# Kernel optimization log

Measured on AMD Instinct MI355X. Metric: run time of the kernel, lower is better.

Reference implementation:

```python
import jax, jax.numpy as jnp
import numpy as np

N, LQ, C, M, L, P = 8, 2048, 256, 8, 4, 4
DH = C // M  # 32
LENS = (2048, 1024, 512, 256)


def setup_inputs() -> dict:
    key = jax.random.key(0)
    ks = jax.random.split(key, 8)
    s = 1.0 / np.sqrt(C)
    return {
        "query": jax.random.normal(ks[0], (N, LQ, C), jnp.float32),
        "reference_points": jax.random.uniform(ks[1], (N, LQ, L, 1), jnp.float32),
        "input_flatten": jax.random.normal(ks[2], (N, sum(LENS), C), jnp.float32),
        "temporal_lens": np.array(LENS, np.int64),
        "level_start_index": np.array([0, 2048, 3072, 3584], np.int64),
        "W_off": jax.random.normal(ks[3], (C, M * L * P), jnp.float32) * 0.01,
        "b_off": jax.random.normal(ks[4], (M * L * P,), jnp.float32),
        "W_attn": jax.random.normal(ks[5], (C, M * L * P), jnp.float32) * 0.01,
        "b_attn": jnp.zeros((M * L * P,), jnp.float32),
        "W_val": jax.random.normal(ks[6], (C, C), jnp.float32) * s,
        "b_val": jnp.zeros((C,), jnp.float32),
        "W_out": jax.random.normal(ks[7], (C, C), jnp.float32) * s,
        "b_out": jnp.zeros((C,), jnp.float32),
    }


def _deform_core(value, lens, loc, attn):
    # value: (N, S, M, DH); loc, attn: (N, LQ, M, L, P); loc in normalized [0,1] coords.
    # Equivalent to per-level F.grid_sample (bilinear, zeros padding, align_corners=False)
    # on a 1xT image: pixel position = loc*T - 0.5; the y-coord 0.5 lands exactly on row 0.
    outs = []
    start = 0
    for l, T in enumerate(lens):
        v = value[:, start:start + T].transpose(0, 2, 1, 3)  # (N, M, T, DH)
        start += T
        pos = loc[..., l, :] * T - 0.5                       # (N, LQ, M, P)
        x0f = jnp.floor(pos)
        frac = pos - x0f
        x0 = x0f.astype(jnp.int32)

        def gather(idx):
            i = jnp.clip(idx, 0, T - 1).transpose(0, 2, 1, 3).reshape(N, M, LQ * P, 1)
            return jnp.take_along_axis(v, i, axis=2).reshape(N, M, LQ, P, DH)

        in0 = ((x0 >= 0) & (x0 < T)).astype(value.dtype)
        in1 = ((x0 + 1 >= 0) & (x0 + 1 < T)).astype(value.dtype)
        w0 = ((1.0 - frac) * in0).transpose(0, 2, 1, 3)[..., None]  # (N, M, LQ, P, 1)
        w1 = (frac * in1).transpose(0, 2, 1, 3)[..., None]
        outs.append(gather(x0) * w0 + gather(x0 + 1) * w1)          # (N, M, LQ, P, DH)
    sampled = jnp.stack(outs, axis=3)          # (N, M, LQ, L, P, DH)
    aw = attn.transpose(0, 2, 1, 3, 4)         # (N, M, LQ, L, P)
    return jnp.einsum('nmqlpd,nmqlp->nqmd', sampled, aw).reshape(N, LQ, C)


def reference(query, reference_points, input_flatten, temporal_lens, level_start_index,
              W_off, b_off, W_attn, b_attn, W_val, b_val, W_out, b_out):
    lens = [int(t) for t in np.asarray(temporal_lens)[:L]]  # static per-level lengths
    value = (input_flatten @ W_val + b_val).reshape(N, -1, M, DH)
    off = (query @ W_off + b_off).reshape(N, LQ, M, L, P)
    attn = jax.nn.softmax((query @ W_attn + b_attn).reshape(N, LQ, M, L * P), axis=-1)
    attn = attn.reshape(N, LQ, M, L, P)
    norm = jnp.asarray(lens, query.dtype)                    # offset_normalizer (L,)
    loc = reference_points[:, :, None, :, None, 0] + off / norm[None, None, None, :, None]
    out = _deform_core(value, lens, loc, attn)
    out = out @ W_out + b_out
    return out, loc, attn
```

## Files before the change

### kernel.cpp

```cpp
#include <hip/hip_runtime.h>
#include <hip/hip_bf16.h>
#include <math.h>

#define NB 8
#define LQ 2048
#define SSUM 3840

typedef unsigned short ushort_t;
typedef unsigned int uint_t;
typedef __attribute__((ext_vector_type(8))) short bf16x8;
typedef __attribute__((ext_vector_type(4))) float f32x4;

__device__ __forceinline__ ushort_t f2bf(float f) {
  __hip_bfloat16 h = __float2bfloat16(f);
  return *reinterpret_cast<ushort_t*>(&h);
}
__device__ __forceinline__ uint_t pk2bf(float lo, float hi) {
  float2 t; t.x = lo; t.y = hi;
  __hip_bfloat162 h = __float22bfloat162_rn(t);
  return *reinterpret_cast<uint_t*>(&h);
}
__device__ __forceinline__ float bf2f_lo(uint_t u) {
  union { uint_t u32; float f; } x;
  x.u32 = u << 16;
  return x.f;
}
__device__ __forceinline__ float bf2f_hi(uint_t u) {
  union { uint_t u32; float f; } x;
  x.u32 = u & 0xffff0000u;
  return x.f;
}
__device__ __forceinline__ void ld_lds16(const void* g, void* l) {
  __builtin_amdgcn_global_load_lds(
      (const __attribute__((address_space(1))) void*)g,
      (__attribute__((address_space(3))) void*)l, 16, 0, 0);
}

__global__ __launch_bounds__(256) void prep(
    const float* __restrict__ W_val, const float* __restrict__ W_off,
    const float* __restrict__ W_attn, const float* __restrict__ W_out,
    ushort_t* __restrict__ BtVal, ushort_t* __restrict__ BtOA,
    ushort_t* __restrict__ BtOut) {
  const int b = blockIdx.x, t = threadIdx.x;
  if (b < 256) { BtVal[b * 256 + t] = f2bf(W_val[(size_t)t * 256 + b]); return; }
  if (b < 512) { int n = b - 256; BtOut[n * 256 + t] = f2bf(W_out[(size_t)t * 256 + n]); return; }
  if (b < 640) { int n = b - 512; BtOA[n * 256 + t] = f2bf(W_off[(size_t)t * 128 + n]); return; }
  int n = b - 640; BtOA[(128 + n) * 256 + t] = f2bf(W_attn[(size_t)t * 128 + n]);
}

template <bool AF32>
__global__ __launch_bounds__(256) void gemm_fused(
    int job_base,
    const float* __restrict__ in_flat, const float* __restrict__ query,
    const ushort_t* __restrict__ core,
    const ushort_t* __restrict__ BtVal, const ushort_t* __restrict__ BtOA,
    const ushort_t* __restrict__ BtOut,
    const float* __restrict__ b_val, const float* __restrict__ b_off,
    const float* __restrict__ b_attn, const float* __restrict__ b_out,
    ushort_t* __restrict__ value, float* __restrict__ loc,
    float* __restrict__ attn, float* __restrict__ out) {
  __shared__ ushort_t Ab[2][64][32];
  __shared__ ushort_t Bb[2][256][32];

  const int job = job_base + blockIdx.x;

  const float* Afp = nullptr;
  const ushort_t* Abf = nullptr;
  const ushort_t* Bt;
  const float* bias_lo; const float* bias_hi;
  int bm, cstride;
  ushort_t* Cb = nullptr;
  float* Cf_lo = nullptr; float* Cf_hi = nullptr;

  if (job < 480) {
    bm = job * 64; Afp = in_flat; Bt = BtVal;
    bias_lo = b_val; bias_hi = b_val + 128; Cb = value; cstride = 256;
  } else if (job < 736) {
    bm = (job - 480) * 64; Afp = query; Bt = BtOA;
    bias_lo = b_off; bias_hi = b_attn; Cf_lo = loc; Cf_hi = attn; cstride = 128;
  } else {
    bm = (job - 736) * 64; Abf = core; Bt = BtOut;
    bias_lo = b_out; bias_hi = b_out + 128; Cf_lo = out; Cf_hi = out + 128;
    cstride = 256;
  }

  const int tid = threadIdx.x;
  const int lane = tid & 63;
  const int wv = tid >> 6;
  const int quad = lane >> 4;
  const int l16 = lane & 15;
  const int wm = (wv >> 1) * 32;
  const int wn = (wv & 1) * 128;
  const int drow = lane >> 2;
  const int dk = (lane & 3) * 8;

  const int asr = tid >> 2;
  const int ask = (tid & 3) * 8;

  f32x4 acc[2][8];
#pragma unroll
  for (int i = 0; i < 2; ++i)
#pragma unroll
    for (int j = 0; j < 8; ++j) acc[i][j] = (f32x4)(0.f);

  auto stageB = [&](int db, int k0) {
#pragma unroll
    for (int c = 0; c < 4; ++c)
      ld_lds16(Bt + (size_t)(wv * 64 + c * 16 + drow) * 256 + k0 + dk,
               &Bb[db][wv * 64 + c * 16 + drow][dk]);
  };
  auto stageA_dma = [&](int db, int k0) {
    ld_lds16(Abf + (size_t)(bm + wv * 16 + drow) * 256 + k0 + dk,
             &Ab[db][wv * 16 + drow][dk]);
  };
  auto stageA_f32 = [&](int db, int k0) {
    const float* gp = Afp + (size_t)(bm + asr) * 256 + k0 + ask;
    float4 f0 = *(const float4*)gp;
    float4 f1 = *(const float4*)(gp + 4);
    uint4 c;
    c.x = pk2bf(f0.x, f0.y);
    c.y = pk2bf(f0.z, f0.w);
    c.z = pk2bf(f1.x, f1.y);
    c.w = pk2bf(f1.z, f1.w);
    *(uint4*)&Ab[db][asr][ask] = c;
  };

  if (AF32) stageA_f32(0, 0); else stageA_dma(0, 0);
  stageB(0, 0);

#pragma unroll
  for (int it = 0; it < 8; ++it) {
    const int db = it & 1;
    __syncthreads();
    if (it < 7) {
      if (AF32) stageA_f32(db ^ 1, (it + 1) * 32); else stageA_dma(db ^ 1, (it + 1) * 32);
      stageB(db ^ 1, (it + 1) * 32);
    }
    bf16x8 af[2], bfr[8];
#pragma unroll
    for (int mi = 0; mi < 2; ++mi)
      af[mi] = *(const bf16x8*)&Ab[db][wm + mi * 16 + l16][quad * 8];
#pragma unroll
    for (int ni = 0; ni < 8; ++ni)
      bfr[ni] = *(const bf16x8*)&Bb[db][wn + ni * 16 + l16][quad * 8];
#pragma unroll
    for (int mi = 0; mi < 2; ++mi)
#pragma unroll
      for (int ni = 0; ni < 8; ++ni)
        acc[mi][ni] = __builtin_amdgcn_mfma_f32_16x16x32_bf16(af[mi], bfr[ni], acc[mi][ni], 0, 0, 0);
  }

  const int hi = wv & 1;
  const float* bias = hi ? bias_hi : bias_lo;
  ushort_t* Cbw = Cb ? (Cb + (hi ? 128 : 0)) : nullptr;
  float* Cfw = hi ? Cf_hi : Cf_lo;

#pragma unroll
  for (int ni = 0; ni < 8; ++ni) {
    int cc = ni * 16 + l16;
    float bv = bias[cc];
#pragma unroll
    for (int mi = 0; mi < 2; ++mi) {
      f32x4 v = acc[mi][ni];
      int rbase = bm + wm + mi * 16 + quad * 4;
#pragma unroll
      for (int r = 0; r < 4; ++r) {
        float o = v[r] + bv;
        size_t idx = (size_t)(rbase + r) * cstride + cc;
        if (Cbw) Cbw[idx] = f2bf(o);
        else     Cfw[idx] = o;
      }
    }
  }
}

__global__ __launch_bounds__(256) void deform_fused(
    const ushort_t* __restrict__ value,
    float* __restrict__ locbuf,
    float* __restrict__ attnbuf,
    const float* __restrict__ refp,
    ushort_t* __restrict__ core) {
  const int tid = threadIdx.x;
  const int nq0 = blockIdx.x * 4;
  const int n = nq0 >> 11;

  __shared__ float slv[512];
  __shared__ float slog[512];
  __shared__ float4 sp[512];

  const float rnorm[4] = {1.f / 2048.f, 1.f / 1024.f, 1.f / 512.f, 1.f / 256.f};
  const int lensA[4] = {2048, 1024, 512, 256};
  const int startsA[4] = {0, 2048, 3072, 3584};

#pragma unroll
  for (int j = 0; j < 2; ++j) {
    int s = tid + j * 256;
    int q = s >> 7;
    int r = s & 127;
    int l = (r >> 2) & 3;
    float lv = refp[(size_t)(nq0 + q) * 4 + l] +
               locbuf[(size_t)nq0 * 128 + s] * rnorm[l];
    locbuf[(size_t)nq0 * 128 + s] = lv;
    slv[s] = lv;
    slog[s] = attnbuf[(size_t)nq0 * 128 + s];
  }
  __syncthreads();

  if (tid < 32) {
    int base = tid * 16;
    float v[16];
#pragma unroll
    for (int i = 0; i < 16; ++i) v[i] = slog[base + i];
    float mx = v[0];
#pragma unroll
    for (int i = 1; i < 16; ++i) mx = fmaxf(mx, v[i]);
    float ssum = 0.f;
#pragma unroll
    for (int i = 0; i < 16; ++i) { v[i] = __expf(v[i] - mx); ssum += v[i]; }
    float rs = 1.f / ssum;
    float* gout = attnbuf + (size_t)nq0 * 128 + base;
#pragma unroll
    for (int i = 0; i < 16; ++i) {
      float pv = v[i] * rs;
      slog[base + i] = pv;
      gout[i] = pv;
    }
  }
  __syncthreads();

#pragma unroll
  for (int j = 0; j < 2; ++j) {
    int s = tid + j * 256;
    int q = s >> 7;
    int r = s & 127;
    int m = r >> 4;
    int lp = r & 15;
    int l = lp >> 2;
    int T = lensA[l];
    float lv = slv[s];
    float aw = slog[s];
    float pos = lv * (float)T - 0.5f;
    float x0f = floorf(pos);
    float fr = pos - x0f;
    int x0 = (int)x0f;
    float w0 = ((unsigned)x0 < (unsigned)T) ? (1.f - fr) * aw : 0.f;
    float w1 = ((unsigned)(x0 + 1) < (unsigned)T) ? fr * aw : 0.f;
    int i0 = min(max(x0, 0), T - 1);
    int i1 = min(max(x0 + 1, 0), T - 1);
    float4 pr;
    pr.x = w0;
    pr.y = w1;
    pr.z = __int_as_float((startsA[l] + i0) * 256);
    pr.w = __int_as_float((startsA[l] + i1) * 256);
    sp[q * 128 + lp * 8 + m] = pr;
  }
  __syncthreads();

  const int q = tid >> 6;
  const int t64 = tid & 63;
  const int m = t64 >> 3;
  const int g = t64 & 7;
  const ushort_t* vbase = value + (size_t)n * (SSUM * 256) + m * 32 + g * 4;

  float a0 = 0.f, a1 = 0.f, a2 = 0.f, a3 = 0.f;
#pragma unroll
  for (int lp = 0; lp < 16; ++lp) {
    float4 pr = sp[q * 128 + lp * 8 + m];
    int o0 = __float_as_int(pr.z);
    int o1 = __float_as_int(pr.w);
    uint2 u0 = *(const uint2*)(vbase + o0);
    uint2 u1 = *(const uint2*)(vbase + o1);
    a0 += pr.x * bf2f_lo(u0.x) + pr.y * bf2f_lo(u1.x);
    a1 += pr.x * bf2f_hi(u0.x) + pr.y * bf2f_hi(u1.x);
    a2 += pr.x * bf2f_lo(u0.y) + pr.y * bf2f_lo(u1.y);
    a3 += pr.x * bf2f_hi(u0.y) + pr.y * bf2f_hi(u1.y);
  }
  uint2 outp;
  outp.x = (uint_t)f2bf(a0) | ((uint_t)f2bf(a1) << 16);
  outp.y = (uint_t)f2bf(a2) | ((uint_t)f2bf(a3) << 16);
  *(uint2*)&core[(size_t)(nq0 + q) * 256 + m * 32 + g * 4] = outp;
}

extern "C" void kernel_launch(void* const* d_in, const int* in_sizes, int n_in,
                              void* d_out, int out_size, void* d_ws, size_t ws_size,
                              hipStream_t stream) {
  const float* query    = (const float*)d_in[0];
  const float* refpts   = (const float*)d_in[1];
  const float* in_flat  = (const float*)d_in[2];
  const float* W_off  = (const float*)d_in[5];
  const float* b_off  = (const float*)d_in[6];
  const float* W_attn = (const float*)d_in[7];
  const float* b_attn = (const float*)d_in[8];
  const float* W_val  = (const float*)d_in[9];
  const float* b_val  = (const float*)d_in[10];
  const float* W_out  = (const float*)d_in[11];
  const float* b_out  = (const float*)d_in[12];

  float* out  = (float*)d_out;
  float* loc  = out + (size_t)NB * LQ * 256;
  float* attn = loc + (size_t)NB * LQ * 128;

  ushort_t* value = (ushort_t*)d_ws;
  ushort_t* core  = value + (size_t)NB * SSUM * 256;
  ushort_t* BtVal = core + (size_t)NB * LQ * 256;
  ushort_t* BtOA  = BtVal + 65536;
  ushort_t* BtOut = BtOA + 65536;

  const int Mq = NB * LQ;

  prep<<<768, 256, 0, stream>>>(W_val, W_off, W_attn, W_out, BtVal, BtOA, BtOut);

  gemm_fused<true><<<736, 256, 0, stream>>>(
      0, in_flat, query, core, BtVal, BtOA, BtOut,
      b_val, b_off, b_attn, b_out, value, loc, attn, out);

  deform_fused<<<Mq / 4, 256, 0, stream>>>(value, loc, attn, refpts, core);

  gemm_fused<false><<<256, 256, 0, stream>>>(
      736, in_flat, query, core, BtVal, BtOA, BtOut,
      b_val, b_off, b_attn, b_out, value, loc, attn, out);
}
```

Measured before the change: 164.7 us.

## Fuse loc/softmax epilogue into GEMM and XOR-swizzle LDS tiles

Moves the sampling-location computation (reference point plus normalized offset) and the per-head softmax of attention logits into the epilogue of the offset/attention GEMM. The softmax uses wave shuffles across the 16 columns of each head. This removes a global read-modify-write pass and two barriers from the deform kernel. It also applies an XOR swizzle to the LDS layout of the A and B tiles to reduce bank conflicts on the MFMA fragment loads. The trade-off is more shuffles and exp work in the GEMM epilogue and more complex address math.

```diff
diff --git a/kernel.cpp b/kernel.cpp
--- a/kernel.cpp
+++ b/kernel.cpp
@@ -57,6 +57,7 @@
     const ushort_t* __restrict__ BtOut,
     const float* __restrict__ b_val, const float* __restrict__ b_off,
     const float* __restrict__ b_attn, const float* __restrict__ b_out,
+    const float* __restrict__ refp,
     ushort_t* __restrict__ value, float* __restrict__ loc,
     float* __restrict__ attn, float* __restrict__ out) {
   __shared__ ushort_t Ab[2][64][32];
@@ -68,17 +69,20 @@
   const ushort_t* Abf = nullptr;
   const ushort_t* Bt;
   const float* bias_lo; const float* bias_hi;
-  int bm, cstride;
+  int bm, cstride, jt;
   ushort_t* Cb = nullptr;
   float* Cf_lo = nullptr; float* Cf_hi = nullptr;
 
   if (job < 480) {
+    jt = 0;
     bm = job * 64; Afp = in_flat; Bt = BtVal;
     bias_lo = b_val; bias_hi = b_val + 128; Cb = value; cstride = 256;
   } else if (job < 736) {
+    jt = 1;
     bm = (job - 480) * 64; Afp = query; Bt = BtOA;
     bias_lo = b_off; bias_hi = b_attn; Cf_lo = loc; Cf_hi = attn; cstride = 128;
   } else {
+    jt = 2;
     bm = (job - 736) * 64; Abf = core; Bt = BtOut;
     bias_lo = b_out; bias_hi = b_out + 128; Cf_lo = out; Cf_hi = out + 128;
     cstride = 256;
@@ -93,9 +97,13 @@
   const int wn = (wv & 1) * 128;
   const int drow = lane >> 2;
   const int dk = (lane & 3) * 8;
+  const int dks = (((lane & 3) ^ ((drow >> 1) & 3)) * 8);
 
   const int asr = tid >> 2;
   const int ask = (tid & 3) * 8;
+  const int askw = (((tid & 3) ^ ((asr >> 1) & 3)) * 8);
+
+  const int qk = ((quad ^ ((l16 >> 1) & 3)) * 8);
 
   f32x4 acc[2][8];
 #pragma unroll
@@ -106,11 +114,11 @@
   auto stageB = [&](int db, int k0) {
 #pragma unroll
     for (int c = 0; c < 4; ++c)
-      ld_lds16(Bt + (size_t)(wv * 64 + c * 16 + drow) * 256 + k0 + dk,
+      ld_lds16(Bt + (size_t)(wv * 64 + c * 16 + drow) * 256 + k0 + dks,
                &Bb[db][wv * 64 + c * 16 + drow][dk]);
   };
   auto stageA_dma = [&](int db, int k0) {
-    ld_lds16(Abf + (size_t)(bm + wv * 16 + drow) * 256 + k0 + dk,
+    ld_lds16(Abf + (size_t)(bm + wv * 16 + drow) * 256 + k0 + dks,
              &Ab[db][wv * 16 + drow][dk]);
   };
   auto stageA_f32 = [&](int db, int k0) {
@@ -122,7 +130,7 @@
     c.y = pk2bf(f0.z, f0.w);
     c.z = pk2bf(f1.x, f1.y);
     c.w = pk2bf(f1.z, f1.w);
-    *(uint4*)&Ab[db][asr][ask] = c;
+    *(uint4*)&Ab[db][asr][askw] = c;
   };
 
   if (AF32) stageA_f32(0, 0); else stageA_dma(0, 0);
@@ -139,10 +147,10 @@
     bf16x8 af[2], bfr[8];
 #pragma unroll
     for (int mi = 0; mi < 2; ++mi)
-      af[mi] = *(const bf16x8*)&Ab[db][wm + mi * 16 + l16][quad * 8];
+      af[mi] = *(const bf16x8*)&Ab[db][wm + mi * 16 + l16][qk];
 #pragma unroll
     for (int ni = 0; ni < 8; ++ni)
-      bfr[ni] = *(const bf16x8*)&Bb[db][wn + ni * 16 + l16][quad * 8];
+      bfr[ni] = *(const bf16x8*)&Bb[db][wn + ni * 16 + l16][qk];
 #pragma unroll
     for (int mi = 0; mi < 2; ++mi)
 #pragma unroll
@@ -152,81 +160,86 @@
 
   const int hi = wv & 1;
   const float* bias = hi ? bias_hi : bias_lo;
-  ushort_t* Cbw = Cb ? (Cb + (hi ? 128 : 0)) : nullptr;
-  float* Cfw = hi ? Cf_hi : Cf_lo;
-
-#pragma unroll
-  for (int ni = 0; ni < 8; ++ni) {
-    int cc = ni * 16 + l16;
-    float bv = bias[cc];
-#pragma unroll
-    for (int mi = 0; mi < 2; ++mi) {
-      f32x4 v = acc[mi][ni];
-      int rbase = bm + wm + mi * 16 + quad * 4;
-#pragma unroll
-      for (int r = 0; r < 4; ++r) {
-        float o = v[r] + bv;
-        size_t idx = (size_t)(rbase + r) * cstride + cc;
-        if (Cbw) Cbw[idx] = f2bf(o);
-        else     Cfw[idx] = o;
+
+  if (jt == 1) {
+    if (!hi) {
+      const int l = l16 >> 2;
+      const float rn = (float)(1 << l) * (1.0f / 2048.0f);
+#pragma unroll
+      for (int mi = 0; mi < 2; ++mi) {
+        int rbase = bm + wm + mi * 16 + quad * 4;
+#pragma unroll
+        for (int r = 0; r < 4; ++r) {
+          int row = rbase + r;
+          float rp = refp[(size_t)row * 4 + l];
+#pragma unroll
+          for (int ni = 0; ni < 8; ++ni) {
+            int cc = ni * 16 + l16;
+            float o = acc[mi][ni][r] + bias[cc];
+            loc[(size_t)row * 128 + cc] = fmaf(o, rn, rp);
+          }
+        }
+      }
+    } else {
+#pragma unroll
+      for (int mi = 0; mi < 2; ++mi) {
+        int rbase = bm + wm + mi * 16 + quad * 4;
+#pragma unroll
+        for (int r = 0; r < 4; ++r) {
+          int row = rbase + r;
+#pragma unroll
+          for (int ni = 0; ni < 8; ++ni) {
+            int cc = ni * 16 + l16;
+            float x = acc[mi][ni][r] + bias[cc];
+            float mx = x;
+            mx = fmaxf(mx, __shfl_xor(mx, 1, 64));
+            mx = fmaxf(mx, __shfl_xor(mx, 2, 64));
+            mx = fmaxf(mx, __shfl_xor(mx, 4, 64));
+            mx = fmaxf(mx, __shfl_xor(mx, 8, 64));
+            float e = __expf(x - mx);
+            float sm = e;
+            sm += __shfl_xor(sm, 1, 64);
+            sm += __shfl_xor(sm, 2, 64);
+            sm += __shfl_xor(sm, 4, 64);
+            sm += __shfl_xor(sm, 8, 64);
+            attn[(size_t)row * 128 + cc] = e / sm;
+          }
+        }
       }
     }
+  } else {
+    ushort_t* Cbw = Cb ? (Cb + (hi ? 128 : 0)) : nullptr;
+    float* Cfw = hi ? Cf_hi : Cf_lo;
+#pragma unroll
+    for (int ni = 0; ni < 8; ++ni) {
+      int cc = ni * 16 + l16;
+      float bv = bias[cc];
+#pragma unroll
+      for (int mi = 0; mi < 2; ++mi) {
+        f32x4 v = acc[mi][ni];
+        int rbase = bm + wm + mi * 16 + quad * 4;
+#pragma unroll
+        for (int r = 0; r < 4; ++r) {
+          float o = v[r] + bv;
+          size_t idx = (size_t)(rbase + r) * cstride + cc;
+          if (Cbw) Cbw[idx] = f2bf(o);
+          else     Cfw[idx] = o;
+        }
+      }
+    }
   }
 }
 
 __global__ __launch_bounds__(256) void deform_fused(
     const ushort_t* __restrict__ value,
-    float* __restrict__ locbuf,
-    float* __restrict__ attnbuf,
-    const float* __restrict__ refp,
+    const float* __restrict__ locbuf,
+    const float* __restrict__ attnbuf,
     ushort_t* __restrict__ core) {
   const int tid = threadIdx.x;
   const int nq0 = blockIdx.x * 4;
   const int n = nq0 >> 11;
 
-  __shared__ float slv[512];
-  __shared__ float slog[512];
   __shared__ float4 sp[512];
-
-  const float rnorm[4] = {1.f / 2048.f, 1.f / 1024.f, 1.f / 512.f, 1.f / 256.f};
-  const int lensA[4] = {2048, 1024, 512, 256};
-  const int startsA[4] = {0, 2048, 3072, 3584};
-
-#pragma unroll
-  for (int j = 0; j < 2; ++j) {
-    int s = tid + j * 256;
-    int q = s >> 7;
-    int r = s & 127;
-    int l = (r >> 2) & 3;
-    float lv = refp[(size_t)(nq0 + q) * 4 + l] +
-               locbuf[(size_t)nq0 * 128 + s] * rnorm[l];
-    locbuf[(size_t)nq0 * 128 + s] = lv;
-    slv[s] = lv;
-    slog[s] = attnbuf[(size_t)nq0 * 128 + s];
-  }
-  __syncthreads();
-
-  if (tid < 32) {
-    int base = tid * 16;
-    float v[16];
-#pragma unroll
-    for (int i = 0; i < 16; ++i) v[i] = slog[base + i];
-    float mx = v[0];
-#pragma unroll
-    for (int i = 1; i < 16; ++i) mx = fmaxf(mx, v[i]);
-    float ssum = 0.f;
-#pragma unroll
-    for (int i = 0; i < 16; ++i) { v[i] = __expf(v[i] - mx); ssum += v[i]; }
-    float rs = 1.f / ssum;
-    float* gout = attnbuf + (size_t)nq0 * 128 + base;
-#pragma unroll
-    for (int i = 0; i < 16; ++i) {
-      float pv = v[i] * rs;
-      slog[base + i] = pv;
-      gout[i] = pv;
-    }
-  }
-  __syncthreads();
 
 #pragma unroll
   for (int j = 0; j < 2; ++j) {
@@ -236,9 +249,10 @@
     int m = r >> 4;
     int lp = r & 15;
     int l = lp >> 2;
-    int T = lensA[l];
-    float lv = slv[s];
-    float aw = slog[s];
+    int T = 2048 >> l;
+    int start = 4096 - (4096 >> l);
+    float lv = locbuf[(size_t)nq0 * 128 + s];
+    float aw = attnbuf[(size_t)nq0 * 128 + s];
     float pos = lv * (float)T - 0.5f;
     float x0f = floorf(pos);
     float fr = pos - x0f;
@@ -250,8 +264,8 @@
     float4 pr;
     pr.x = w0;
     pr.y = w1;
-    pr.z = __int_as_float((startsA[l] + i0) * 256);
-    pr.w = __int_as_float((startsA[l] + i1) * 256);
+    pr.z = __int_as_float((start + i0) * 256);
+    pr.w = __int_as_float((start + i1) * 256);
     sp[q * 128 + lp * 8 + m] = pr;
   }
   __syncthreads();
@@ -312,11 +326,11 @@
 
   gemm_fused<true><<<736, 256, 0, stream>>>(
       0, in_flat, query, core, BtVal, BtOA, BtOut,
-      b_val, b_off, b_attn, b_out, value, loc, attn, out);
-
-  deform_fused<<<Mq / 4, 256, 0, stream>>>(value, loc, attn, refpts, core);
+      b_val, b_off, b_attn, b_out, refpts, value, loc, attn, out);
+
+  deform_fused<<<Mq / 4, 256, 0, stream>>>(value, loc, attn, core);
 
   gemm_fused<false><<<256, 256, 0, stream>>>(
       736, in_flat, query, core, BtVal, BtOA, BtOut,
-      b_val, b_off, b_attn, b_out, value, loc, attn, out);
-}
+      b_val, b_off, b_attn, b_out, refpts, value, loc, attn, out);
+}
```

New measurement: 191.1 us. 1.16x slower.

## Pre-convert GEMM inputs to bf16 and use a 3-stage DMA pipeline

Applied to the files above, without the earlier changes.

The weight-prep kernel now also converts in_flat and query from fp32 to bf16, writing them into the value and core workspace buffers. This lets every GEMM job stage its A tile with direct global-to-LDS loads. The GEMM moves from two LDS buffers to a triple-buffered pipeline that uses explicit vmcnt waits and barriers. In the deform kernel the softmax is done with wave shuffles in registers, replacing the shared-memory pass and two block barriers. The trade-off is an extra full read and write of the inputs in bf16, plus in-place reuse of workspace buffers, in exchange for smoother GEMM loads.

```diff
diff --git a/kernel.cpp b/kernel.cpp
--- a/kernel.cpp
+++ b/kernel.cpp
@@ -36,36 +36,51 @@
       (__attribute__((address_space(3))) void*)l, 16, 0, 0);
 }
 
-__global__ __launch_bounds__(256) void prep(
+__global__ __launch_bounds__(256) void prep_conv(
     const float* __restrict__ W_val, const float* __restrict__ W_off,
     const float* __restrict__ W_attn, const float* __restrict__ W_out,
+    const float* __restrict__ in_flat, const float* __restrict__ query,
     ushort_t* __restrict__ BtVal, ushort_t* __restrict__ BtOA,
-    ushort_t* __restrict__ BtOut) {
+    ushort_t* __restrict__ BtOut,
+    ushort_t* in_bf, ushort_t* q_bf) {
   const int b = blockIdx.x, t = threadIdx.x;
-  if (b < 256) { BtVal[b * 256 + t] = f2bf(W_val[(size_t)t * 256 + b]); return; }
-  if (b < 512) { int n = b - 256; BtOut[n * 256 + t] = f2bf(W_out[(size_t)t * 256 + n]); return; }
-  if (b < 640) { int n = b - 512; BtOA[n * 256 + t] = f2bf(W_off[(size_t)t * 128 + n]); return; }
-  int n = b - 640; BtOA[(128 + n) * 256 + t] = f2bf(W_attn[(size_t)t * 128 + n]);
-}
-
-template <bool AF32>
+  if (b < 768) {
+    if (b < 256) { BtVal[b * 256 + t] = f2bf(W_val[(size_t)t * 256 + b]); return; }
+    if (b < 512) { int n = b - 256; BtOut[n * 256 + t] = f2bf(W_out[(size_t)t * 256 + n]); return; }
+    if (b < 640) { int n = b - 512; BtOA[n * 256 + t] = f2bf(W_off[(size_t)t * 128 + n]); return; }
+    int n = b - 640; BtOA[(128 + n) * 256 + t] = f2bf(W_attn[(size_t)t * 128 + n]);
+    return;
+  }
+  size_t gid = (size_t)(b - 768) * 256 + t;
+  const float* src; ushort_t* dst; size_t e;
+  if (gid < 983040u) { src = in_flat; dst = in_bf; e = gid * 8; }
+  else               { src = query;   dst = q_bf;  e = (gid - 983040u) * 8; }
+  float4 f0 = *(const float4*)(src + e);
+  float4 f1 = *(const float4*)(src + e + 4);
+  uint4 c;
+  c.x = pk2bf(f0.x, f0.y);
+  c.y = pk2bf(f0.z, f0.w);
+  c.z = pk2bf(f1.x, f1.y);
+  c.w = pk2bf(f1.z, f1.w);
+  *(uint4*)(dst + e) = c;
+}
+
 __global__ __launch_bounds__(256) void gemm_fused(
     int job_base,
-    const float* __restrict__ in_flat, const float* __restrict__ query,
-    const ushort_t* __restrict__ core,
+    const ushort_t* in_bf,
+    const ushort_t* qcore,
     const ushort_t* __restrict__ BtVal, const ushort_t* __restrict__ BtOA,
     const ushort_t* __restrict__ BtOut,
     const float* __restrict__ b_val, const float* __restrict__ b_off,
     const float* __restrict__ b_attn, const float* __restrict__ b_out,
-    ushort_t* __restrict__ value, float* __restrict__ loc,
+    ushort_t* value, float* __restrict__ loc,
     float* __restrict__ attn, float* __restrict__ out) {
-  __shared__ ushort_t Ab[2][64][32];
-  __shared__ ushort_t Bb[2][256][32];
+  __shared__ ushort_t Ab[3][64][32];
+  __shared__ ushort_t Bb[3][256][32];
 
   const int job = job_base + blockIdx.x;
 
-  const float* Afp = nullptr;
-  const ushort_t* Abf = nullptr;
+  const ushort_t* Asrc;
   const ushort_t* Bt;
   const float* bias_lo; const float* bias_hi;
   int bm, cstride;
@@ -73,13 +88,13 @@
   float* Cf_lo = nullptr; float* Cf_hi = nullptr;
 
   if (job < 480) {
-    bm = job * 64; Afp = in_flat; Bt = BtVal;
+    bm = job * 64; Asrc = in_bf; Bt = BtVal;
     bias_lo = b_val; bias_hi = b_val + 128; Cb = value; cstride = 256;
   } else if (job < 736) {
-    bm = (job - 480) * 64; Afp = query; Bt = BtOA;
+    bm = (job - 480) * 64; Asrc = qcore; Bt = BtOA;
     bias_lo = b_off; bias_hi = b_attn; Cf_lo = loc; Cf_hi = attn; cstride = 128;
   } else {
-    bm = (job - 736) * 64; Abf = core; Bt = BtOut;
+    bm = (job - 736) * 64; Asrc = qcore; Bt = BtOut;
     bias_lo = b_out; bias_hi = b_out + 128; Cf_lo = out; Cf_hi = out + 128;
     cstride = 256;
   }
@@ -94,55 +109,40 @@
   const int drow = lane >> 2;
   const int dk = (lane & 3) * 8;
 
-  const int asr = tid >> 2;
-  const int ask = (tid & 3) * 8;
-
   f32x4 acc[2][8];
 #pragma unroll
   for (int i = 0; i < 2; ++i)
 #pragma unroll
     for (int j = 0; j < 8; ++j) acc[i][j] = (f32x4)(0.f);
 
-  auto stageB = [&](int db, int k0) {
+  auto stage = [&](int sb, int k0) {
+    ld_lds16(Asrc + (size_t)(bm + wv * 16 + drow) * 256 + k0 + dk,
+             &Ab[sb][wv * 16 + drow][dk]);
 #pragma unroll
     for (int c = 0; c < 4; ++c)
       ld_lds16(Bt + (size_t)(wv * 64 + c * 16 + drow) * 256 + k0 + dk,
-               &Bb[db][wv * 64 + c * 16 + drow][dk]);
+               &Bb[sb][wv * 64 + c * 16 + drow][dk]);
   };
-  auto stageA_dma = [&](int db, int k0) {
-    ld_lds16(Abf + (size_t)(bm + wv * 16 + drow) * 256 + k0 + dk,
-             &Ab[db][wv * 16 + drow][dk]);
-  };
-  auto stageA_f32 = [&](int db, int k0) {
-    const float* gp = Afp + (size_t)(bm + asr) * 256 + k0 + ask;
-    float4 f0 = *(const float4*)gp;
-    float4 f1 = *(const float4*)(gp + 4);
-    uint4 c;
-    c.x = pk2bf(f0.x, f0.y);
-    c.y = pk2bf(f0.z, f0.w);
-    c.z = pk2bf(f1.x, f1.y);
-    c.w = pk2bf(f1.z, f1.w);
-    *(uint4*)&Ab[db][asr][ask] = c;
-  };
-
-  if (AF32) stageA_f32(0, 0); else stageA_dma(0, 0);
-  stageB(0, 0);
+
+  stage(0, 0);
+  stage(1, 32);
 
 #pragma unroll
   for (int it = 0; it < 8; ++it) {
-    const int db = it & 1;
-    __syncthreads();
-    if (it < 7) {
-      if (AF32) stageA_f32(db ^ 1, (it + 1) * 32); else stageA_dma(db ^ 1, (it + 1) * 32);
-      stageB(db ^ 1, (it + 1) * 32);
-    }
+    if (it < 7) asm volatile("s_waitcnt vmcnt(5)" ::: "memory");
+    else        asm volatile("s_waitcnt vmcnt(0)" ::: "memory");
+    __builtin_amdgcn_s_barrier();
+    __builtin_amdgcn_sched_barrier(0);
+    if (it < 6) stage((it + 2) % 3, (it + 2) * 32);
+
+    const int sb = it % 3;
     bf16x8 af[2], bfr[8];
 #pragma unroll
     for (int mi = 0; mi < 2; ++mi)
-      af[mi] = *(const bf16x8*)&Ab[db][wm + mi * 16 + l16][quad * 8];
+      af[mi] = *(const bf16x8*)&Ab[sb][wm + mi * 16 + l16][quad * 8];
 #pragma unroll
     for (int ni = 0; ni < 8; ++ni)
-      bfr[ni] = *(const bf16x8*)&Bb[db][wn + ni * 16 + l16][quad * 8];
+      bfr[ni] = *(const bf16x8*)&Bb[sb][wn + ni * 16 + l16][quad * 8];
 #pragma unroll
     for (int mi = 0; mi < 2; ++mi)
 #pragma unroll
@@ -184,49 +184,7 @@
   const int nq0 = blockIdx.x * 4;
   const int n = nq0 >> 11;
 
-  __shared__ float slv[512];
-  __shared__ float slog[512];
   __shared__ float4 sp[512];
-
-  const float rnorm[4] = {1.f / 2048.f, 1.f / 1024.f, 1.f / 512.f, 1.f / 256.f};
-  const int lensA[4] = {2048, 1024, 512, 256};
-  const int startsA[4] = {0, 2048, 3072, 3584};
-
-#pragma unroll
-  for (int j = 0; j < 2; ++j) {
-    int s = tid + j * 256;
-    int q = s >> 7;
-    int r = s & 127;
-    int l = (r >> 2) & 3;
-    float lv = refp[(size_t)(nq0 + q) * 4 + l] +
-               locbuf[(size_t)nq0 * 128 + s] * rnorm[l];
-    locbuf[(size_t)nq0 * 128 + s] = lv;
-    slv[s] = lv;
-    slog[s] = attnbuf[(size_t)nq0 * 128 + s];
-  }
-  __syncthreads();
-
-  if (tid < 32) {
-    int base = tid * 16;
-    float v[16];
-#pragma unroll
-    for (int i = 0; i < 16; ++i) v[i] = slog[base + i];
-    float mx = v[0];
-#pragma unroll
-    for (int i = 1; i < 16; ++i) mx = fmaxf(mx, v[i]);
-    float ssum = 0.f;
-#pragma unroll
-    for (int i = 0; i < 16; ++i) { v[i] = __expf(v[i] - mx); ssum += v[i]; }
-    float rs = 1.f / ssum;
-    float* gout = attnbuf + (size_t)nq0 * 128 + base;
-#pragma unroll
-    for (int i = 0; i < 16; ++i) {
-      float pv = v[i] * rs;
-      slog[base + i] = pv;
-      gout[i] = pv;
-    }
-  }
-  __syncthreads();
 
 #pragma unroll
   for (int j = 0; j < 2; ++j) {
@@ -236,9 +194,29 @@
     int m = r >> 4;
     int lp = r & 15;
     int l = lp >> 2;
-    int T = lensA[l];
-    float lv = slv[s];
-    float aw = slog[s];
+    int T = 2048 >> l;
+    int start = 4096 - (4096 >> l);
+    float rn = (float)(1 << l) * (1.0f / 2048.0f);
+
+    float lraw = locbuf[(size_t)nq0 * 128 + s];
+    float logit = attnbuf[(size_t)nq0 * 128 + s];
+    float lv = refp[(size_t)(nq0 + q) * 4 + l] + lraw * rn;
+    locbuf[(size_t)nq0 * 128 + s] = lv;
+
+    float mx = logit;
+    mx = fmaxf(mx, __shfl_xor(mx, 1, 64));
+    mx = fmaxf(mx, __shfl_xor(mx, 2, 64));
+    mx = fmaxf(mx, __shfl_xor(mx, 4, 64));
+    mx = fmaxf(mx, __shfl_xor(mx, 8, 64));
+    float e = __expf(logit - mx);
+    float sm = e;
+    sm += __shfl_xor(sm, 1, 64);
+    sm += __shfl_xor(sm, 2, 64);
+    sm += __shfl_xor(sm, 4, 64);
+    sm += __shfl_xor(sm, 8, 64);
+    float aw = e / sm;
+    attnbuf[(size_t)nq0 * 128 + s] = aw;
+
     float pos = lv * (float)T - 0.5f;
     float x0f = floorf(pos);
     float fr = pos - x0f;
@@ -250,8 +228,8 @@
     float4 pr;
     pr.x = w0;
     pr.y = w1;
-    pr.z = __int_as_float((startsA[l] + i0) * 256);
-    pr.w = __int_as_float((startsA[l] + i1) * 256);
+    pr.z = __int_as_float((start + i0) * 256);
+    pr.w = __int_as_float((start + i1) * 256);
     sp[q * 128 + lp * 8 + m] = pr;
   }
   __syncthreads();
@@ -308,15 +286,17 @@
 
   const int Mq = NB * LQ;
 
-  prep<<<768, 256, 0, stream>>>(W_val, W_off, W_attn, W_out, BtVal, BtOA, BtOut);
-
-  gemm_fused<true><<<736, 256, 0, stream>>>(
-      0, in_flat, query, core, BtVal, BtOA, BtOut,
+  prep_conv<<<768 + 5888, 256, 0, stream>>>(
+      W_val, W_off, W_attn, W_out, in_flat, query,
+      BtVal, BtOA, BtOut, value, core);
+
+  gemm_fused<<<736, 256, 0, stream>>>(
+      0, value, core, BtVal, BtOA, BtOut,
       b_val, b_off, b_attn, b_out, value, loc, attn, out);
 
   deform_fused<<<Mq / 4, 256, 0, stream>>>(value, loc, attn, refpts, core);
 
-  gemm_fused<false><<<256, 256, 0, stream>>>(
-      736, in_flat, query, core, BtVal, BtOA, BtOut,
+  gemm_fused<<<256, 256, 0, stream>>>(
+      736, value, core, BtVal, BtOA, BtOut,
       b_val, b_off, b_attn, b_out, value, loc, attn, out);
 }
```

Result: slower. 168.5 us (+2.3%).
